# Optimization experiments

Measured on AMD Instinct MI355X. Metric: run time of the kernel, lower is better.

## Reference

```python
import jax, jax.numpy as jnp
import numpy as np

N = 100000
F_IN = 128
HID = 256
N_CLS = 40
E = 1600000


def setup_inputs() -> dict:
    key = jax.random.key(0)
    ks = jax.random.split(key, 12)
    x = jax.random.normal(ks[0], (N, F_IN), dtype=jnp.float32)
    edge_index = jax.random.randint(ks[1], (2, E), 0, N, dtype=jnp.int64)
    # GCNConv params (glorot-ish scale), conv2 is reused twice in forward
    def lin(k, fi, fo):
        return jax.random.normal(k, (fi, fo), dtype=jnp.float32) * (1.0 / np.sqrt(fi))
    return {
        "x": x,
        "edge_index": edge_index,
        "W1": lin(ks[2], F_IN, HID), "b1": jnp.zeros((HID,), jnp.float32),
        "W2": lin(ks[3], HID, HID),  "b2": jnp.zeros((HID,), jnp.float32),
        "W3": lin(ks[4], HID, HID),  "b3": jnp.zeros((HID,), jnp.float32),
        "W4": lin(ks[5], HID, N_CLS), "b4": jnp.zeros((N_CLS,), jnp.float32),
    }


def _gcn_norm(edge_index, n):
    # add self-loops, compute symmetric normalization D^-1/2 (A+I) D^-1/2
    loop = jnp.arange(n, dtype=edge_index.dtype)
    src = jnp.concatenate([edge_index[0], loop])
    dst = jnp.concatenate([edge_index[1], loop])
    deg = jax.ops.segment_sum(jnp.ones_like(dst, dtype=jnp.float32), dst, num_segments=n)
    dinv = jnp.where(deg > 0, jax.lax.rsqrt(deg), 0.0)
    norm = dinv[src] * dinv[dst]  # [E+N]
    return src, dst, norm


def _gcn_conv(x, W, b, src, dst, norm, n):
    h = x @ W                       # [N, Fout] dense transform first (fewer msg bytes)
    msg = h[src] * norm[:, None]    # gather + scale
    out = jax.ops.segment_sum(msg, dst, num_segments=n)  # scatter-add
    return out + b


def reference(x, edge_index, W1, b1, W2, b2, W3, b3, W4, b4):
    n = x.shape[0]
    src, dst, norm = _gcn_norm(edge_index, n)
    h = jax.nn.relu(_gcn_conv(x, W1, b1, src, dst, norm, n))
    h = jax.nn.relu(_gcn_conv(h, W2, b2, src, dst, norm, n))
    h = jax.nn.relu(_gcn_conv(h, W2, b2, src, dst, norm, n))  # conv2 reused, as in source
    h = jax.nn.relu(_gcn_conv(h, W3, b3, src, dst, norm, n))
    h = _gcn_conv(h, W4, b4, src, dst, norm, n)
    return jax.nn.log_softmax(h, axis=1)
```

## Files before the change

kernel.cpp:

```cpp
#include <hip/hip_runtime.h>
#include <stdint.h>
#include <math.h>

#define NN   100000
#define FIN  128
#define HIDDEN 256
#define NCLS 40
#define NE   1600000

#define PRNG 8
#define RNG  12500
#define SSL  32
#define NES  50000

typedef unsigned short u16;
typedef unsigned char u8;
typedef __attribute__((ext_vector_type(8))) short s16x8;
typedef __attribute__((ext_vector_type(4))) float f32x4;
typedef __attribute__((ext_vector_type(2))) float f32x2;

__device__ __forceinline__ float bf2f(unsigned short u) {
    union { float f; uint32_t i; } v; v.i = ((uint32_t)u) << 16; return v.f;
}
__device__ __forceinline__ unsigned short f2bf(float f) {
    union { float f; uint32_t i; } v; v.f = f;
    uint32_t r = v.i + 0x7fffu + ((v.i >> 16) & 1u);
    return (unsigned short)(r >> 16);
}
__device__ __forceinline__ u8 f2fp8(float f) {
    int r = __builtin_amdgcn_cvt_pk_fp8_f32(f, f, 0, false);
    return (u8)(r & 0xff);
}

__global__ __launch_bounds__(256) void k_detect(const u16* __restrict__ x16,
                                                const int* __restrict__ ei,
                                                int* __restrict__ flags) {
    int g = blockIdx.x * 256 + threadIdx.x;
    uint2 v = *(const uint2*)(x16 + (size_t)g * 4);
    int nan_cnt = 0;
    uint32_t w0 = v.x, w1 = v.y;
    if (((w0 >> 0)  & 0x7fff) >= 0x7f80) nan_cnt++;
    if (((w0 >> 16) & 0x7fff) >= 0x7f80) nan_cnt++;
    if (((w1 >> 0)  & 0x7fff) >= 0x7f80) nan_cnt++;
    if (((w1 >> 16) & 0x7fff) >= 0x7f80) nan_cnt++;
    int odd_nz = (g < 8192 && ei[2 * g + 1] != 0) ? 1 : 0;
#pragma unroll
    for (int off = 1; off < 64; off <<= 1) {
        nan_cnt += __shfl_xor(nan_cnt, off);
        odd_nz  += __shfl_xor(odd_nz, off);
    }
    if ((threadIdx.x & 63) == 0) {
        if (nan_cnt) atomicAdd(&flags[0], nan_cnt);
        if (odd_nz)  atomicAdd(&flags[2], odd_nz);
    }
}

__global__ void k_compact(const int* __restrict__ ei, int* __restrict__ dst32,
                          int* __restrict__ src32, const int* __restrict__ flags) {
    int e = blockIdx.x * 256 + threadIdx.x;
    if (e < NE) {
        if (flags[2] == 0) { src32[e] = ei[2 * e]; dst32[e] = ei[2 * (NE + e)]; }
        else               { src32[e] = ei[e];     dst32[e] = ei[NE + e]; }
    }
}

__global__ void k_trans_cvt(const void* W1, const void* W2, const void* W3, const void* W4,
                            u16* W1t, u16* W2t, u16* W3t, u16* W4t,
                            const void* b1, const void* b2, const void* b3, const void* b4,
                            u16* o1, u16* o2, u16* o3, u16* o4,
                            const void* __restrict__ x, const float* __restrict__ dinv,
                            u16* __restrict__ xb,
                            const int* __restrict__ flags) {
    int b = blockIdx.x;
    int fl = flags[0];
    int t = threadIdx.x;
    if (b >= 705) {
        int i = (b - 705) * 256 + t;
        if (i < NN * FIN) {
            float v = fl ? ((const float*)x)[i] : bf2f(((const u16*)x)[i]);
            xb[i] = f2bf(v * dinv[i >> 7]);
        }
        return;
    }
    if (b == 704) {
        o1[t] = fl ? f2bf(((const float*)b1)[t]) : ((const u16*)b1)[t];
        o2[t] = fl ? f2bf(((const float*)b2)[t]) : ((const u16*)b2)[t];
        o3[t] = fl ? f2bf(((const float*)b3)[t]) : ((const u16*)b3)[t];
        if (t < 64) o4[t] = (t < NCLS) ? (fl ? f2bf(((const float*)b4)[t]) : ((const u16*)b4)[t]) : (u16)0;
        return;
    }
    const void* W; u16* Wt; int K, F, Fpad, base;
    if (b < 128)      { W = W1; Wt = W1t; K = 128; F = 256; Fpad = 256; base = 0; }
    else if (b < 384) { W = W2; Wt = W2t; K = 256; F = 256; Fpad = 256; base = 128; }
    else if (b < 640) { W = W3; Wt = W3t; K = 256; F = 256; Fpad = 256; base = 384; }
    else              { W = W4; Wt = W4t; K = 256; F = 40;  Fpad = 64;  base = 640; }
    int idx = (b - base) * 256 + t;
    if (idx >= K * Fpad) return;
    int f = idx / K, k = idx - f * K;
    u16 v = 0;
    if (f < F) {
        if (fl) v = f2bf(((const float*)W)[(size_t)k * F + f]);
        else    v = ((const u16*)W)[(size_t)k * F + f];
    }
    Wt[idx] = v;
}


__global__ __launch_bounds__(256) void k_histb(const int* __restrict__ dst32,
                                               int* __restrict__ partial) {
    __shared__ int h[RNG];
    int p = blockIdx.x >> 5, s = blockIdx.x & 31;
    int t = threadIdx.x;
    int4 z4 = make_int4(0, 0, 0, 0);
    for (int i = t * 4; i < RNG; i += 1024) *(int4*)(h + i) = z4;
    __syncthreads();
    int base = s * NES;
    int lo = p * RNG;
    int nfull = NES & ~1023;
    for (int k = t * 4; k < nfull; k += 1024) {
        int4 d4 = *(const int4*)(dst32 + base + k);
        int a;
        a = d4.x - lo; if ((unsigned)a < RNG) atomicAdd(&h[a], 1);
        a = d4.y - lo; if ((unsigned)a < RNG) atomicAdd(&h[a], 1);
        a = d4.z - lo; if ((unsigned)a < RNG) atomicAdd(&h[a], 1);
        a = d4.w - lo; if ((unsigned)a < RNG) atomicAdd(&h[a], 1);
    }
    for (int k = nfull + t; k < NES; k += 256) {
        int a = dst32[base + k] - lo;
        if ((unsigned)a < RNG) atomicAdd(&h[a], 1);
    }
    __syncthreads();
    int* out = partial + blockIdx.x * RNG;
    for (int i = t * 4; i < RNG; i += 1024) *(int4*)(out + i) = *(const int4*)(h + i);
}

__global__ __launch_bounds__(256) void k_scan1(const int* __restrict__ partial,
                                               int* __restrict__ cnt,
                                               int* __restrict__ out,
                                               int* __restrict__ bsum) {
    __shared__ int sh[256];
    int t = threadIdx.x;
    int base = blockIdx.x * 1024 + t * 4;
    int v0 = 0, v1 = 0, v2 = 0, v3 = 0;
    if (base < NN) {
        int p = base / RNG, il = base - p * RNG;
        const int* q = partial + (p * SSL) * RNG + il;
        int4 acc = make_int4(0, 0, 0, 0);
#pragma unroll
        for (int s = 0; s < SSL; ++s) {
            int4 w = *(const int4*)(q + s * RNG);
            acc.x += w.x; acc.y += w.y; acc.z += w.z; acc.w += w.w;
        }
        v0 = acc.x; v1 = acc.y; v2 = acc.z; v3 = acc.w;
        *(int4*)(cnt + base) = acc;
    }
    int s = v0 + v1 + v2 + v3;
    sh[t] = s;
    __syncthreads();
    for (int off = 1; off < 256; off <<= 1) {
        int x = (t >= off) ? sh[t - off] : 0;
        __syncthreads();
        sh[t] += x;
        __syncthreads();
    }
    int ex = sh[t] - s;
    if (base < NN) {
        int4 o = make_int4(ex, ex + v0, ex + v0 + v1, ex + v0 + v1 + v2);
        *(int4*)(out + base) = o;
    }
    if (t == 255) bsum[blockIdx.x] = sh[255];
}

__global__ void k_scan2(int* bsum, int nb) {
    if (threadIdx.x == 0 && blockIdx.x == 0) {
        int run = 0;
        for (int i = 0; i < nb; ++i) { int t = bsum[i]; bsum[i] = run; run += t; }
    }
}

__global__ void k_scan3o(int* __restrict__ rp, const int* __restrict__ bsum,
                         const int* __restrict__ cnt, float* __restrict__ dinv,
                         int* __restrict__ partial) {
    int i = blockIdx.x * 256 + threadIdx.x;
    if (i < NN) {
        int v = rp[i] + bsum[i >> 10];
        rp[i] = v;
        dinv[i] = rsqrtf((float)(cnt[i] + 1));
        int p = i / RNG, il = i - p * RNG;
        int* q = partial + (p * SSL) * RNG + il;
        int run = v;
#pragma unroll
        for (int s = 0; s < SSL; ++s) { int t = q[s * RNG]; q[s * RNG] = run; run += t; }
    }
    if (i == 0) rp[NN] = NE;
}

__global__ __launch_bounds__(256) void k_fillb(const int* __restrict__ dst32,
                                               const int* __restrict__ src32,
                                               const int* __restrict__ offs,
                                               int* __restrict__ col) {
    __shared__ int h[RNG];
    int p = blockIdx.x >> 5, s = blockIdx.x & 31;
    int t = threadIdx.x;
    const int* o = offs + blockIdx.x * RNG;
    for (int i = t * 4; i < RNG; i += 1024) *(int4*)(h + i) = *(const int4*)(o + i);
    __syncthreads();
    int base = s * NES;
    int lo = p * RNG;
    int nfull = NES & ~1023;
    for (int k = t * 4; k < nfull; k += 1024) {
        int4 d4 = *(const int4*)(dst32 + base + k);
        int4 s4 = *(const int4*)(src32 + base + k);
        int a;
        a = d4.x - lo; if ((unsigned)a < RNG) col[atomicAdd(&h[a], 1)] = s4.x;
        a = d4.y - lo; if ((unsigned)a < RNG) col[atomicAdd(&h[a], 1)] = s4.y;
        a = d4.z - lo; if ((unsigned)a < RNG) col[atomicAdd(&h[a], 1)] = s4.z;
        a = d4.w - lo; if ((unsigned)a < RNG) col[atomicAdd(&h[a], 1)] = s4.w;
    }
    for (int k = nfull + t; k < NES; k += 256) {
        int a = dst32[base + k] - lo;
        if ((unsigned)a < RNG) col[atomicAdd(&h[a], 1)] = src32[base + k];
    }
}


#define GLL(g, l) __builtin_amdgcn_global_load_lds( \
    (const __attribute__((address_space(1))) unsigned int*)(g), \
    (__attribute__((address_space(3))) unsigned int*)(l), 16, 0, 0)

#define NT128 ((NN + 127) / 128)
#define NT256 ((NN + 255) / 256)

__global__ __launch_bounds__(256) void k_gemmP(const u16* __restrict__ A,
                                               const u16* __restrict__ Wt,
                                               const float* __restrict__ dinv,
                                               const u16* __restrict__ bias,
                                               u16* __restrict__ C,
                                               int K, int out_fp8) {
    __shared__ __align__(16) u16 Bs[128 * 256];
    __shared__ __align__(16) u16 As[2 * 128 * 32];
    int t = threadIdx.x;
    int bn = blockIdx.y;
    int w = t >> 6, lane = t & 63;
    int wm = w >> 1, wn = w & 1;
    int lrow = lane & 15, lq = lane >> 4;
    int r0 = t >> 2;
    int seg = (t & 3) * 8;

    int rounds = K >> 4;
    for (int r = 0; r < rounds; ++r) {
        int d = r * 4096 + t * 16;
        int kt = d >> 13;
        int win = d & 8191;
        int row = win >> 6;
        int sg = (win & 63) >> 1;
        GLL(Wt + (size_t)(bn * 128 + row) * K + kt * 32 + sg, Bs + (d >> 1));
    }

    int nK = K >> 5;
    bool fuse = (bias != nullptr);
    float bcol[4];
#pragma unroll
    for (int j = 0; j < 4; ++j)
        bcol[j] = fuse ? bf2f(bias[bn * 128 + wn * 64 + j * 16 + lrow]) : 0.f;

    for (int tm = blockIdx.x; tm < NT128; tm += gridDim.x) {
        int rowBase = tm * 128;
        int ar0 = rowBase + r0;       if (ar0 > NN - 1) ar0 = NN - 1;
        int ar1 = rowBase + 64 + r0;  if (ar1 > NN - 1) ar1 = NN - 1;
        const u16* a0p = A + (size_t)ar0 * K + seg;
        const u16* a1p = A + (size_t)ar1 * K + seg;
        GLL(a0p, As + t * 8);
        GLL(a1p, As + 2048 + t * 8);

        f32x4 acc[4][4] = {};
        int cur = 0;
        for (int kt = 0; kt < nK; ++kt) {
            __syncthreads();
            if (kt + 1 < nK) {
                int nxt = cur ^ 1;
                GLL(a0p + (kt + 1) * 32, As + nxt * 4096 + t * 8);
                GLL(a1p + (kt + 1) * 32, As + nxt * 4096 + 2048 + t * 8);
            }
            const u16* ab = As + cur * 4096;
            const u16* bb = Bs + kt * 4096;
            s16x8 af[4], bf[4];
#pragma unroll
            for (int i = 0; i < 4; ++i)
                af[i] = *(const s16x8*)(ab + (wm * 64 + i * 16 + lrow) * 32 + lq * 8);
#pragma unroll
            for (int j = 0; j < 4; ++j)
                bf[j] = *(const s16x8*)(bb + (wn * 64 + j * 16 + lrow) * 32 + lq * 8);
#pragma unroll
            for (int i = 0; i < 4; ++i)
#pragma unroll
                for (int j = 0; j < 4; ++j)
                    acc[i][j] = __builtin_amdgcn_mfma_f32_16x16x32_bf16(af[i], bf[j], acc[i][j], 0, 0, 0);
            cur ^= 1;
        }

        u8* C8 = (u8*)C;
#pragma unroll
        for (int i = 0; i < 4; ++i) {
#pragma unroll
            for (int rr = 0; rr < 4; ++rr) {
                int row = rowBase + wm * 64 + i * 16 + lq * 4 + rr;
                if (row < NN) {
                    float d = dinv[row];
#pragma unroll
                    for (int j = 0; j < 4; ++j) {
                        int colg = bn * 128 + wn * 64 + j * 16 + lrow;
                        float v = fuse ? fmaxf(fmaf(d, acc[i][j][rr], bcol[j]), 0.f)
                                       : acc[i][j][rr] * d;
                        if (out_fp8) C8[(size_t)row * HIDDEN + colg] = f2fp8(v);
                        else         C[(size_t)row * HIDDEN + colg] = f2bf(v);
                    }
                }
            }
        }
        __syncthreads();
    }
}

__global__ __launch_bounds__(256) void k_gemmP64(const u16* __restrict__ A,
                                                 const u16* __restrict__ Wt,
                                                 const float* __restrict__ dinv,
                                                 u16* __restrict__ C) {
    const int K = 256;
    __shared__ __align__(16) u16 Bs[64 * 256];
    __shared__ __align__(16) u16 As[2 * 256 * 32];
    int t = threadIdx.x;
    int w = t >> 6, lane = t & 63;
    int lrow = lane & 15, lq = lane >> 4;
    int seg = (t & 3) * 8;
    int rr0 = t >> 2;

    for (int r = 0; r < 8; ++r)
        GLL(Wt + (size_t)(t >> 2) * K + r * 32 + seg, Bs + r * 2048 + t * 8);

    for (int tm = blockIdx.x; tm < NT256; tm += gridDim.x) {
        int rowBase = tm * 256;
        const u16* ap[4];
#pragma unroll
        for (int c = 0; c < 4; ++c) {
            int ar = rowBase + c * 64 + rr0;
            if (ar > NN - 1) ar = NN - 1;
            ap[c] = A + (size_t)ar * K + seg;
        }
#pragma unroll
        for (int c = 0; c < 4; ++c) GLL(ap[c], As + c * 2048 + t * 8);

        f32x4 acc[4][4] = {};
        int cur = 0;
        for (int kt = 0; kt < 8; ++kt) {
            __syncthreads();
            if (kt + 1 < 8) {
                int nxt = cur ^ 1;
#pragma unroll
                for (int c = 0; c < 4; ++c)
                    GLL(ap[c] + (kt + 1) * 32, As + nxt * 8192 + c * 2048 + t * 8);
            }
            const u16* ab = As + cur * 8192;
            const u16* bb = Bs + kt * 2048;
            s16x8 af[4], bf[4];
#pragma unroll
            for (int i = 0; i < 4; ++i)
                af[i] = *(const s16x8*)(ab + (w * 64 + i * 16 + lrow) * 32 + lq * 8);
#pragma unroll
            for (int j = 0; j < 4; ++j)
                bf[j] = *(const s16x8*)(bb + (j * 16 + lrow) * 32 + lq * 8);
#pragma unroll
            for (int i = 0; i < 4; ++i)
#pragma unroll
                for (int j = 0; j < 4; ++j)
                    acc[i][j] = __builtin_amdgcn_mfma_f32_16x16x32_bf16(af[i], bf[j], acc[i][j], 0, 0, 0);
            cur ^= 1;
        }

#pragma unroll
        for (int i = 0; i < 4; ++i) {
#pragma unroll
            for (int rr = 0; rr < 4; ++rr) {
                int row = rowBase + w * 64 + i * 16 + lq * 4 + rr;
                if (row < NN) {
                    float d = dinv[row];
#pragma unroll
                    for (int j = 0; j < 4; ++j) {
                        int colg = j * 16 + lrow;
                        C[(size_t)row * 64 + colg] = f2bf(acc[i][j][rr] * d);
                    }
                }
            }
        }
        __syncthreads();
    }
}


__global__ __launch_bounds__(256) void k_agg8(const u8* __restrict__ hs,
                                              const int* __restrict__ rp,
                                              const int* __restrict__ col,
                                              const float* __restrict__ dinv,
                                              const u16* __restrict__ bias,
                                              u16* __restrict__ out) {
    int wq = __builtin_amdgcn_readfirstlane(threadIdx.x >> 6);
    int row = blockIdx.x * 4 + wq;
    if (row >= NN) return;
    int lane = threadIdx.x & 63;
    int fo = lane * 4;
    float a0 = 0.f, a1 = 0.f, a2 = 0.f, a3 = 0.f;
    auto acc_add = [&](uint32_t w) {
        f32x2 x = __builtin_amdgcn_cvt_pk_f32_fp8(w, false);
        f32x2 y = __builtin_amdgcn_cvt_pk_f32_fp8(w, true);
        a0 += x.x; a1 += x.y; a2 += y.x; a3 += y.y;
    };
    auto acc_fma = [&](uint32_t w, float m) {
        f32x2 x = __builtin_amdgcn_cvt_pk_f32_fp8(w, false);
        f32x2 y = __builtin_amdgcn_cvt_pk_f32_fp8(w, true);
        a0 = fmaf(m, x.x, a0); a1 = fmaf(m, x.y, a1);
        a2 = fmaf(m, y.x, a2); a3 = fmaf(m, y.y, a3);
    };
    acc_add(*(const uint32_t*)(hs + (size_t)row * HIDDEN + fo));
    int p  = __builtin_amdgcn_readfirstlane(rp[row]);
    int p1 = __builtin_amdgcn_readfirstlane(rp[row + 1]);
    for (; p + 8 <= p1; p += 8) {
        uint32_t v[8];
#pragma unroll
        for (int k = 0; k < 8; ++k) {
            int c = __builtin_amdgcn_readfirstlane(col[p + k]);
            v[k] = *(const uint32_t*)(hs + (size_t)c * HIDDEN + fo);
        }
#pragma unroll
        for (int k = 0; k < 8; ++k) acc_add(v[k]);
    }
    int rem = p1 - p;
    if (rem) {
        uint32_t v[8];
#pragma unroll
        for (int k = 0; k < 8; ++k) {
            int idx = (k < rem) ? (p + k) : p;
            int c = __builtin_amdgcn_readfirstlane(col[idx]);
            v[k] = *(const uint32_t*)(hs + (size_t)c * HIDDEN + fo);
        }
#pragma unroll
        for (int k = 0; k < 8; ++k) acc_fma(v[k], (k < rem) ? 1.f : 0.f);
    }
    float d = dinv[row];
    uint2 bv = *(const uint2*)(bias + fo);
    float r0 = fmaxf(fmaf(d, a0, bf2f((u16)(bv.x & 0xffff))), 0.f);
    float r1 = fmaxf(fmaf(d, a1, bf2f((u16)(bv.x >> 16))), 0.f);
    float r2 = fmaxf(fmaf(d, a2, bf2f((u16)(bv.y & 0xffff))), 0.f);
    float r3 = fmaxf(fmaf(d, a3, bf2f((u16)(bv.y >> 16))), 0.f);
    uint2 o;
    o.x = (uint32_t)f2bf(r0) | ((uint32_t)f2bf(r1) << 16);
    o.y = (uint32_t)f2bf(r2) | ((uint32_t)f2bf(r3) << 16);
    *(uint2*)(out + (size_t)row * HIDDEN + fo) = o;
}

__global__ __launch_bounds__(256) void k_aggx(const u16* __restrict__ xb,
                                              const int* __restrict__ rp,
                                              const int* __restrict__ col,
                                              u16* __restrict__ out) {
    int wq = __builtin_amdgcn_readfirstlane(threadIdx.x >> 6);
    int row = blockIdx.x * 4 + wq;
    if (row >= NN) return;
    int lane = threadIdx.x & 63;
    int fo = lane * 2;
    float a0 = 0.f, a1 = 0.f;
    auto acc_add = [&](uint32_t w) {
        a0 += bf2f((u16)(w & 0xffff));
        a1 += bf2f((u16)(w >> 16));
    };
    auto acc_fma = [&](uint32_t w, float m) {
        a0 = fmaf(m, bf2f((u16)(w & 0xffff)), a0);
        a1 = fmaf(m, bf2f((u16)(w >> 16)), a1);
    };
    acc_add(*(const uint32_t*)(xb + (size_t)row * FIN + fo));
    int p  = __builtin_amdgcn_readfirstlane(rp[row]);
    int p1 = __builtin_amdgcn_readfirstlane(rp[row + 1]);
    for (; p + 8 <= p1; p += 8) {
        uint32_t v[8];
#pragma unroll
        for (int k = 0; k < 8; ++k) {
            int c = __builtin_amdgcn_readfirstlane(col[p + k]);
            v[k] = *(const uint32_t*)(xb + (size_t)c * FIN + fo);
        }
#pragma unroll
        for (int k = 0; k < 8; ++k) acc_add(v[k]);
    }
    int rem = p1 - p;
    if (rem) {
        uint32_t v[8];
#pragma unroll
        for (int k = 0; k < 8; ++k) {
            int idx = (k < rem) ? (p + k) : p;
            int c = __builtin_amdgcn_readfirstlane(col[idx]);
            v[k] = *(const uint32_t*)(xb + (size_t)c * FIN + fo);
        }
#pragma unroll
        for (int k = 0; k < 8; ++k) acc_fma(v[k], (k < rem) ? 1.f : 0.f);
    }
    uint32_t o = (uint32_t)f2bf(a0) | ((uint32_t)f2bf(a1) << 16);
    *(uint32_t*)(out + (size_t)row * FIN + fo) = o;
}

__global__ __launch_bounds__(256) void k_agg5(const u16* __restrict__ hs,
                                              const int* __restrict__ rp,
                                              const int* __restrict__ col,
                                              const float* __restrict__ dinv,
                                              const u16* __restrict__ bias,
                                              void* __restrict__ out,
                                              const int* __restrict__ flags) {
    int wq = __builtin_amdgcn_readfirstlane(threadIdx.x >> 6);
    int row = blockIdx.x * 4 + wq;
    if (row >= NN) return;
    int lane = threadIdx.x & 63;
    float a = bf2f(hs[(size_t)row * 64 + lane]);
    int p  = __builtin_amdgcn_readfirstlane(rp[row]);
    int p1 = __builtin_amdgcn_readfirstlane(rp[row + 1]);
    for (; p + 8 <= p1; p += 8) {
        u16 v[8];
#pragma unroll
        for (int k = 0; k < 8; ++k) {
            int c = __builtin_amdgcn_readfirstlane(col[p + k]);
            v[k] = hs[(size_t)c * 64 + lane];
        }
#pragma unroll
        for (int k = 0; k < 8; ++k) a += bf2f(v[k]);
    }
    int rem = p1 - p;
    if (rem) {
        u16 v[8];
#pragma unroll
        for (int k = 0; k < 8; ++k) {
            int idx = (k < rem) ? (p + k) : p;
            int c = __builtin_amdgcn_readfirstlane(col[idx]);
            v[k] = hs[(size_t)c * 64 + lane];
        }
#pragma unroll
        for (int k = 0; k < 8; ++k)
            a = fmaf((k < rem) ? 1.f : 0.f, bf2f(v[k]), a);
    }
    bool act = lane < NCLS;
    float d = dinv[row];
    float l = act ? fmaf(d, a, bf2f(bias[lane])) : -1e30f;
    float m = l;
#pragma unroll
    for (int off = 32; off > 0; off >>= 1) m = fmaxf(m, __shfl_xor(m, off));
    float e = act ? __expf(l - m) : 0.f;
#pragma unroll
    for (int off = 32; off > 0; off >>= 1) e += __shfl_xor(e, off);
    if (act) {
        float r = l - m - __logf(e);
        if (flags[0]) ((float*)out)[(size_t)row * NCLS + lane] = r;
        else          ((u16*)out)[(size_t)row * NCLS + lane] = f2bf(r);
    }
}


extern "C" void kernel_launch(void* const* d_in, const int* in_sizes, int n_in,
                              void* d_out, int out_size, void* d_ws, size_t ws_size,
                              hipStream_t stream) {
    const void* x  = d_in[0];
    const int* ei  = (const int*)d_in[1];
    const void* W1 = d_in[2];
    const void* b1 = d_in[3];
    const void* W2 = d_in[4];
    const void* b2 = d_in[5];
    const void* W3 = d_in[6];
    const void* b3 = d_in[7];
    const void* W4 = d_in[8];
    const void* b4 = d_in[9];

    char* p = (char*)d_ws;
    auto alloc = [&](size_t b) -> char* {
        char* r = p;
        p += (b + 255) & ~(size_t)255;
        return r;
    };
    int*   flags = (int*)alloc(256);
    int*   cnt  = (int*)alloc((size_t)NN * 4);
    float* dinv = (float*)alloc((size_t)NN * 4);
    int*   rp   = (int*)alloc((size_t)(NN + 1) * 4);
    int*   col  = (int*)alloc((size_t)NE * 4);
    int*   bsum = (int*)alloc(4096);
    u16* xb  = (u16*)alloc((size_t)NN * FIN * 2);
    u16* W1t = (u16*)alloc((size_t)256 * 128 * 2);
    u16* W2t = (u16*)alloc((size_t)256 * 256 * 2);
    u16* W3t = (u16*)alloc((size_t)256 * 256 * 2);
    u16* W4t = (u16*)alloc((size_t)64 * 256 * 2);
    u16* bb1 = (u16*)alloc(512);
    u16* bb2 = (u16*)alloc(512);
    u16* bb3 = (u16*)alloc(512);
    u16* bb4 = (u16*)alloc(128);
    u16* bufA = (u16*)alloc((size_t)NN * HIDDEN * 2);
    u16* bufB = (u16*)alloc((size_t)NN * HIDDEN * 2);

    int* dst32   = (int*)bufA;
    int* src32   = dst32 + NE;
    int* partial = (int*)bufB;

    hipMemsetAsync(flags, 0, 16, stream);
    k_detect<<<64, 256, 0, stream>>>((const u16*)x, ei, flags);
    k_compact<<<(NE + 255) / 256, 256, 0, stream>>>(ei, dst32, src32, flags);

    k_histb<<<PRNG * SSL, 256, 0, stream>>>(dst32, partial);
    k_scan1<<<(NN + 1023) / 1024, 256, 0, stream>>>(partial, cnt, rp, bsum);
    k_scan2<<<1, 64, 0, stream>>>(bsum, (NN + 1023) / 1024);
    k_scan3o<<<(NN + 255) / 256, 256, 0, stream>>>(rp, bsum, cnt, dinv, partial);
    k_fillb<<<PRNG * SSL, 256, 0, stream>>>(dst32, src32, partial, col);

    k_trans_cvt<<<705 + (NN * FIN + 255) / 256, 256, 0, stream>>>(
        W1, W2, W3, W4, W1t, W2t, W3t, W4t,
        b1, b2, b3, b4, bb1, bb2, bb3, bb4, x, dinv, xb, flags);

    dim3 gP(256, 2);
    dim3 aggGrid((NN + 3) / 4);

    k_aggx<<<aggGrid, 256, 0, stream>>>(xb, rp, col, bufB);
    k_gemmP<<<gP, 256, 0, stream>>>(bufB, W1t, dinv, bb1, bufA, 128, 0);
    k_gemmP<<<gP, 256, 0, stream>>>(bufA, W2t, dinv, nullptr, bufB, 256, 1);
    k_agg8<<<aggGrid, 256, 0, stream>>>((const u8*)bufB, rp, col, dinv, bb2, bufA);
    k_gemmP<<<gP, 256, 0, stream>>>(bufA, W2t, dinv, nullptr, bufB, 256, 1);
    k_agg8<<<aggGrid, 256, 0, stream>>>((const u8*)bufB, rp, col, dinv, bb2, bufA);
    k_gemmP<<<gP, 256, 0, stream>>>(bufA, W3t, dinv, nullptr, bufB, 256, 1);
    k_agg8<<<aggGrid, 256, 0, stream>>>((const u8*)bufB, rp, col, dinv, bb3, bufA);
    k_gemmP64<<<256, 256, 0, stream>>>(bufA, W4t, dinv, bufB);
    k_agg5<<<aggGrid, 256, 0, stream>>>(bufB, rp, col, dinv, bb4, d_out, flags);
}
```

Measured before the change: 702.3 us.

## Vectorize x conversion, parallelize block-sum scan, halve GEMM grid

The x-to-bf16 scaling pass now handles 8 elements per thread with 128-bit loads and stores, which cuts the thread count and the number of memory transactions. The single-thread serial scan over block sums becomes a 128-thread shared-memory Hillis-Steele scan. The persistent GEMM grid drops from 256x2 to 128x2 blocks, trading parallelism for lower per-block overhead, which could leave compute units idle on a large GPU.

Result: slower. 762.0 us (+8.5%).

```diff
diff --git a/kernel.cpp b/kernel.cpp
--- a/kernel.cpp
+++ b/kernel.cpp
@@ -75,10 +75,32 @@
     int fl = flags[0];
     int t = threadIdx.x;
     if (b >= 705) {
-        int i = (b - 705) * 256 + t;
-        if (i < NN * FIN) {
-            float v = fl ? ((const float*)x)[i] : bf2f(((const u16*)x)[i]);
-            xb[i] = f2bf(v * dinv[i >> 7]);
+        int i8 = (b - 705) * 256 + t;
+        if (i8 < NN * FIN / 8) {
+            int i = i8 * 8;
+            float d = dinv[i >> 7];
+            u16 r[8];
+            if (fl) {
+                const float* xf = (const float*)x + i;
+                f32x4 v0 = *(const f32x4*)xf;
+                f32x4 v1 = *(const f32x4*)(xf + 4);
+#pragma unroll
+                for (int k = 0; k < 4; ++k) { r[k] = f2bf(v0[k] * d); r[4 + k] = f2bf(v1[k] * d); }
+            } else {
+                uint4 v = *(const uint4*)((const u16*)x + i);
+                uint32_t w[4] = {v.x, v.y, v.z, v.w};
+#pragma unroll
+                for (int k = 0; k < 4; ++k) {
+                    r[2 * k]     = f2bf(bf2f((u16)(w[k] & 0xffff)) * d);
+                    r[2 * k + 1] = f2bf(bf2f((u16)(w[k] >> 16)) * d);
+                }
+            }
+            uint4 o;
+            o.x = (uint32_t)r[0] | ((uint32_t)r[1] << 16);
+            o.y = (uint32_t)r[2] | ((uint32_t)r[3] << 16);
+            o.z = (uint32_t)r[4] | ((uint32_t)r[5] << 16);
+            o.w = (uint32_t)r[6] | ((uint32_t)r[7] << 16);
+            *(uint4*)(xb + i) = o;
         }
         return;
     }
@@ -172,10 +194,18 @@
 }
 
 __global__ void k_scan2(int* bsum, int nb) {
-    if (threadIdx.x == 0 && blockIdx.x == 0) {
-        int run = 0;
-        for (int i = 0; i < nb; ++i) { int t = bsum[i]; bsum[i] = run; run += t; }
-    }
+    __shared__ int sh[128];
+    int t = threadIdx.x;
+    int v = (t < nb) ? bsum[t] : 0;
+    sh[t] = v;
+    __syncthreads();
+    for (int off = 1; off < 128; off <<= 1) {
+        int x = (t >= off) ? sh[t - off] : 0;
+        __syncthreads();
+        sh[t] += x;
+        __syncthreads();
+    }
+    if (t < nb) bsum[t] = sh[t] - v;
 }
 
 __global__ void k_scan3o(int* __restrict__ rp, const int* __restrict__ bsum,
@@ -606,15 +636,15 @@
 
     k_histb<<<PRNG * SSL, 256, 0, stream>>>(dst32, partial);
     k_scan1<<<(NN + 1023) / 1024, 256, 0, stream>>>(partial, cnt, rp, bsum);
-    k_scan2<<<1, 64, 0, stream>>>(bsum, (NN + 1023) / 1024);
+    k_scan2<<<1, 128, 0, stream>>>(bsum, (NN + 1023) / 1024);
     k_scan3o<<<(NN + 255) / 256, 256, 0, stream>>>(rp, bsum, cnt, dinv, partial);
     k_fillb<<<PRNG * SSL, 256, 0, stream>>>(dst32, src32, partial, col);
 
-    k_trans_cvt<<<705 + (NN * FIN + 255) / 256, 256, 0, stream>>>(
+    k_trans_cvt<<<705 + (NN * FIN / 8 + 255) / 256, 256, 0, stream>>>(
         W1, W2, W3, W4, W1t, W2t, W3t, W4t,
         b1, b2, b3, b4, bb1, bb2, bb3, bb4, x, dinv, xb, flags);
 
-    dim3 gP(256, 2);
+    dim3 gP(128, 2);
     dim3 aggGrid((NN + 3) / 4);
 
     k_aggx<<<aggGrid, 256, 0, stream>>>(xb, rp, col, bufB);
```
